# Optimization experiments

Hardware: AMD Instinct MI355X
Metric: run time of the kernel (lower is better)

Reference implementation:

```python
import jax, jax.numpy as jnp
import numpy as np

N_NODES = 50000
N_EDGES = 800000
N_GRAPHS = 512
K_HOPS = 2


def setup_inputs() -> dict:
    key = jax.random.key(0)
    ks = jax.random.split(key, 6)
    x = jax.random.normal(ks[0], (N_NODES, 75), dtype=jnp.float32)
    edge_index = jax.random.randint(ks[1], (2, N_EDGES), 0, N_NODES, dtype=jnp.int64)
    batch = jnp.sort(jax.random.randint(ks[2], (N_NODES,), 0, N_GRAPHS, dtype=jnp.int64))
    # Glorot-ish init for linear layers
    W1 = jax.random.normal(ks[3], (75, 128), dtype=jnp.float32) * (1.0 / np.sqrt(75))
    b1 = jnp.zeros((128,), dtype=jnp.float32)
    W2 = jax.random.normal(ks[4], (128, 1), dtype=jnp.float32) * (1.0 / np.sqrt(128))
    b2 = jnp.zeros((1,), dtype=jnp.float32)
    return {"x": x, "edge_index": edge_index, "batch": batch,
            "W1": W1, "b1": b1, "W2": W2, "b2": b2}


def _sgc_forward(x, edge_index, batch, W1, b1, W2, b2):
    N = x.shape[0]
    # gcn_norm with added self-loops (PyG SGConv default)
    loop = jnp.arange(N, dtype=edge_index.dtype)
    row = jnp.concatenate([edge_index[0], loop])
    col = jnp.concatenate([edge_index[1], loop])
    w = jnp.ones(row.shape[0], dtype=x.dtype)
    deg = jax.ops.segment_sum(w, col, num_segments=N)
    deg_inv_sqrt = jnp.where(deg > 0, jax.lax.rsqrt(jnp.maximum(deg, 1e-12)), 0.0)
    norm = deg_inv_sqrt[row] * deg_inv_sqrt[col]  # [E+N]
    # K hops of normalized sparse propagation: out[col] += norm * x[row]
    for _ in range(K_HOPS):
        x = jax.ops.segment_sum(norm[:, None] * x[row], col, num_segments=N)
    # SGConv final linear
    h = x @ W1 + b1  # [N,128]
    # global_add_pool: segment sum by graph id
    pooled = jax.ops.segment_sum(h, batch, num_segments=N_GRAPHS)  # [G,128]
    return pooled @ W2 + b2  # [G,1]


def reference(x, edge_index, batch, W1, b1, W2, b2):
    return _sgc_forward(x, edge_index, batch, W1, b1, W2, b2)
```

## Files before the change

kernel.cpp:

```cpp
#include <hip/hip_runtime.h>


#define N_    50000
#define E_    800000
#define G_    512
#define F_    75
#define H_    128
#define RR    256
#define BWR   196
#define PBLK  256
#define EPB   3125
#define SLOT  40
#define NT    196

struct Pr {
    const float* x; const int* row; const int* col; const int* batch;
    const float* W1; const float* b1; const float* W2; const float* b2;
    float* u; float2* kd; float* cbw; int* bcnt; int* bcnt2;
    unsigned* ebuf; unsigned* ebuf2; float* out;
};

__global__ __launch_bounds__(1024)
void k1_part(Pr p) {
    const int t = threadIdx.x, b = blockIdx.x;
    __shared__ float xs[NT * F_];
    __shared__ float sv[F_ + 1];
    __shared__ int wc[RR], wc2[RR];
    if (t < RR) { wc[t] = 0; wc2[t] = 0; }
    if (t < F_) {
        float s = 0.f;
        #pragma unroll 8
        for (int j = 0; j < H_; ++j) s += p.W1[t * H_ + j] * p.W2[j];
        sv[t] = s;
    }
    if (b == 0) {
        if (t >= 512 && t < 1024) p.out[t - 512] = p.b2[0];
        if (t == 500) {
            float s = 0.f;
            #pragma unroll 8
            for (int j = 0; j < H_; ++j) s += p.b1[j] * p.W2[j];
            p.cbw[0] = s;
        }
    }
    const int n0 = b * NT;
    int rem = N_ - n0; if (rem > NT) rem = NT; if (rem < 0) rem = 0;
    const int nf4 = rem * F_ / 4;
    const float4* xsrc = (const float4*)(p.x + (size_t)n0 * F_);
    for (int i = t; i < nf4; i += 1024) ((float4*)xs)[i] = xsrc[i];
    __syncthreads();
    const int e0 = b * EPB;
    for (int e = e0 + t; e < e0 + EPB; e += 1024) {
        int cv = p.col[e];
        int rv = p.row[e];
        int r = cv / BWR;
        int k = atomicAdd(&wc[r], 1);
        if (k < SLOT)
            p.ebuf[(size_t)(r * PBLK + b) * SLOT + k] =
                ((unsigned)rv << 8) | (unsigned)(cv - r * BWR);
        int r2 = rv / BWR;
        int k2 = atomicAdd(&wc2[r2], 1);
        if (k2 < SLOT)
            p.ebuf2[(size_t)(r2 * PBLK + b) * SLOT + k2] =
                ((unsigned)cv << 8) | (unsigned)(rv - r2 * BWR);
    }
    {
        const int ln = t >> 2, part = t & 3;
        if (ln < rem) {
            const float* xr = xs + ln * F_;
            float s = 0.f;
            for (int j = part; j < F_; j += 4) s += xr[j] * sv[j];
            s += __shfl_xor(s, 1);
            s += __shfl_xor(s, 2);
            if (part == 0) p.u[n0 + ln] = s;
        }
    }
    __syncthreads();
    if (t < RR) {
        int c = wc[t];  if (c > SLOT) c = SLOT;
        p.bcnt[t * PBLK + b] = c;
        int c2 = wc2[t]; if (c2 > SLOT) c2 = SLOT;
        p.bcnt2[t * PBLK + b] = c2;
    }
}

__global__ __launch_bounds__(1024)
void k2_deg(Pr p) {
    const int t = threadIdx.x, r = blockIdx.x;
    __shared__ float bins[BWR];
    __shared__ int scnt[PBLK];
    if (t < BWR) bins[t] = 0.f;
    if (t < PBLK) scnt[t] = p.bcnt[r * PBLK + t];
    __syncthreads();
    const int w = t >> 6, lane = t & 63;
    const unsigned* ebr = p.ebuf + (size_t)r * PBLK * SLOT;
    #pragma unroll
    for (int i = 0; i < PBLK / 16; ++i) {
        int b = w * (PBLK / 16) + i;
        if (lane < scnt[b]) {
            unsigned wd = ebr[(size_t)b * SLOT + lane];
            atomicAdd(&bins[wd & 255u], 1.0f);
        }
    }
    __syncthreads();
    if (t < BWR) {
        int node = r * BWR + t;
        if (node < N_) {
            float d = rsqrtf(bins[t] + 1.0f);
            p.kd[node] = make_float2(d, __int_as_float(p.batch[node]));
            p.u[node] = d * p.u[node];
        }
    }
}

__global__ __launch_bounds__(1024)
void k3_hop(Pr p) {
    const int t = threadIdx.x, r = blockIdx.x;
    __shared__ float bins[BWR];
    __shared__ float h[G_];
    __shared__ int scnt[PBLK], scnt2[PBLK];
    if (t < BWR) bins[t] = 0.f;
    for (int i = t; i < G_; i += 1024) h[i] = 0.f;
    if (t < PBLK) {
        scnt[t]  = p.bcnt[r * PBLK + t];
        scnt2[t] = p.bcnt2[r * PBLK + t];
    }
    __syncthreads();
    const int w = t >> 6, lane = t & 63;
    {
        const unsigned* ebr = p.ebuf + (size_t)r * PBLK * SLOT;
        #pragma unroll
        for (int i = 0; i < PBLK / 16; ++i) {
            int b = w * (PBLK / 16) + i;
            if (lane < scnt[b]) {
                unsigned wd = ebr[(size_t)b * SLOT + lane];
                atomicAdd(&bins[wd & 255u], p.u[wd >> 8]);
            }
        }
    }
    __syncthreads();
    if (t < 256) {
        float val = 0.f; int g = -1;
        int node = r * BWR + t;
        if (t < BWR && node < N_) {
            float2 k = p.kd[node];
            float nu = k.x * k.x * (bins[t] + p.u[node]);
            bins[t] = nu;
            val = k.x * nu + p.cbw[0];
            g = __float_as_int(k.y);
        }
        int g0 = __shfl(g, 0), g63 = __shfl(g, 63);
        if (g0 == g63 && g0 >= 0) {
            for (int o = 32; o; o >>= 1) val += __shfl_down(val, o);
            if ((t & 63) == 0) atomicAdd(&h[g0], val);
        } else if (g >= 0) {
            atomicAdd(&h[g], val);
        }
    }
    __syncthreads();
    {
        const unsigned* eb2 = p.ebuf2 + (size_t)r * PBLK * SLOT;
        #pragma unroll
        for (int i = 0; i < PBLK / 16; ++i) {
            int b = w * (PBLK / 16) + i;
            if (lane < scnt2[b]) {
                unsigned wd = eb2[(size_t)b * SLOT + lane];
                float2 k = p.kd[wd >> 8];
                atomicAdd(&h[__float_as_int(k.y)], k.x * bins[wd & 255u]);
            }
        }
    }
    __syncthreads();
    for (int i = t; i < G_; i += 1024)
        if (h[i] != 0.f) atomicAdd(&p.out[i], h[i]);
}

__global__ void f_setup(const float* W1, const float* b1, const float* W2,
                        const float* b2, float* v, float* cb) {
    int t = threadIdx.x;
    if (t < F_) {
        float s = 0.f;
        for (int j = 0; j < H_; ++j) s += W1[t * H_ + j] * W2[j];
        v[t] = s;
    } else if (t == F_) {
        float s = 0.f;
        for (int j = 0; j < H_; ++j) s += b1[j] * W2[j];
        cb[0] = s; cb[1] = b2[0];
    }
}
__global__ void f_init(float* deg, float* s, int n) {
    int i = blockIdx.x * blockDim.x + threadIdx.x;
    if (i < n) { deg[i] = 1.0f; s[i] = 0.0f; }
}
__global__ void f_deg_acc(const int* __restrict__ col, float* deg, int e) {
    int i = blockIdx.x * blockDim.x + threadIdx.x;
    if (i < e) atomicAdd(&deg[col[i]], 1.0f);
}
__global__ void f_dis(float* deg, int n) {
    int i = blockIdx.x * blockDim.x + threadIdx.x;
    if (i < n) deg[i] = rsqrtf(deg[i]);
}
__global__ void f_u0(const float* __restrict__ x, const float* __restrict__ v,
                     const float* __restrict__ dis, float* u, int n) {
    __shared__ float sv[F_];
    if (threadIdx.x < F_) sv[threadIdx.x] = v[threadIdx.x];
    __syncthreads();
    int i = blockIdx.x * blockDim.x + threadIdx.x;
    if (i < n) {
        const float* xi = x + (size_t)i * F_;
        float s = 0.f;
        for (int j = 0; j < F_; ++j) s += xi[j] * sv[j];
        u[i] = dis[i] * s;
    }
}
__global__ void f_edge(const int* __restrict__ row, const int* __restrict__ col,
                       const float* __restrict__ u, float* s, int e) {
    int i = blockIdx.x * blockDim.x + threadIdx.x;
    if (i < e) atomicAdd(&s[col[i]], u[row[i]]);
}
__global__ void f_hop_finish(const float* __restrict__ dis, float* s, float* u, int n) {
    int i = blockIdx.x * blockDim.x + threadIdx.x;
    if (i < n) { float d = dis[i]; u[i] = d * d * (s[i] + u[i]); s[i] = 0.0f; }
}
__global__ void f_out_init(const float* __restrict__ cb, float* out, int g) {
    int i = blockIdx.x * blockDim.x + threadIdx.x;
    if (i < g) out[i] = cb[1];
}
__global__ void f_pool(const int* __restrict__ batch, const float* __restrict__ dis,
                       const float* __restrict__ s, const float* __restrict__ u,
                       const float* __restrict__ cb, float* out, int n) {
    int i = blockIdx.x * blockDim.x + threadIdx.x;
    if (i < n) atomicAdd(&out[batch[i]], dis[i] * (s[i] + u[i]) + cb[0]);
}

extern "C" void kernel_launch(void* const* d_in, const int* in_sizes, int n_in,
                              void* d_out, int out_size, void* d_ws, size_t ws_size,
                              hipStream_t stream) {
    const float* x   = (const float*)d_in[0];
    const int*   ei  = (const int*)d_in[1];
    const int*   bat = (const int*)d_in[2];
    const float* W1  = (const float*)d_in[3];
    const float* b1  = (const float*)d_in[4];
    const float* W2  = (const float*)d_in[5];
    const float* b2  = (const float*)d_in[6];
    float* out = (float*)d_out;

    float* ws = (float*)d_ws;
    Pr p;
    p.x = x; p.row = ei; p.col = ei + E_; p.batch = bat;
    p.W1 = W1; p.b1 = b1; p.W2 = W2; p.b2 = b2;
    p.u     = ws;
    p.kd    = (float2*)(ws + N_ + (N_ & 1));
    p.cbw   = ws + 3 * N_ + 2;
    p.bcnt  = (int*)(p.cbw + 8);
    p.bcnt2 = p.bcnt + RR * PBLK;
    p.ebuf  = (unsigned*)(p.bcnt2 + RR * PBLK);
    p.ebuf2 = p.ebuf + (size_t)RR * PBLK * SLOT;
    p.out   = out;

    const size_t need = ((size_t)3 * N_ + 16 + 2 * (size_t)RR * PBLK * (1 + SLOT))
                        * sizeof(float);

    if (ws_size >= need) {
        k1_part<<<PBLK, 1024, 0, stream>>>(p);
        k2_deg<<<RR, 1024, 0, stream>>>(p);
        k3_hop<<<RR, 1024, 0, stream>>>(p);
    } else {
        float* v  = ws;
        float* cb = ws + 128;
        float* dis = ws + 136;
        float* u  = dis + N_;
        float* s  = u + N_;
        const int B = 256;
        const int gN = (N_ + B - 1) / B;
        const int gE = (E_ + B - 1) / B;
        f_setup<<<1, 128, 0, stream>>>(W1, b1, W2, b2, v, cb);
        f_init<<<gN, B, 0, stream>>>(dis, s, N_);
        f_deg_acc<<<gE, B, 0, stream>>>(ei + E_, dis, E_);
        f_dis<<<gN, B, 0, stream>>>(dis, N_);
        f_u0<<<gN, B, 0, stream>>>(x, v, dis, u, N_);
        f_edge<<<gE, B, 0, stream>>>(ei, ei + E_, u, s, E_);
        f_hop_finish<<<gN, B, 0, stream>>>(dis, s, u, N_);
        f_out_init<<<1, G_, 0, stream>>>(cb, out, G_);
        f_edge<<<gE, B, 0, stream>>>(ei, ei + E_, u, s, E_);
        f_pool<<<gN, B, 0, stream>>>(bat, dis, s, u, cb, out, N_);
    }
}
```

Baseline: 54.90 us.

## Halve partition blocks, widen edge slots, compute node projections directly from global

Reduces the first-pass grid from 256 to 128 blocks, each handling twice as many edges, with 64 bucket slots per destination range instead of 40. The per-node projection of x onto W1·W2 no longer stages x in shared memory; each block instead processes 391 nodes with four threads each reading contiguous chunks straight from global memory. This removes the large shared tile and halves the per-range bucket count the hop kernels must scan, at the cost of fewer blocks, less parallelism in the first kernel, and strided uncoalesced global loads for x.

```diff
diff --git a/kernel.cpp b/kernel.cpp
--- a/kernel.cpp
+++ b/kernel.cpp
@@ -8,10 +8,11 @@
 #define H_    128
 #define RR    256
 #define BWR   196
-#define PBLK  256
-#define EPB   3125
-#define SLOT  40
-#define NT    196
+#define PBLK  128
+#define EPB   6250
+#define SLOT  64
+#define NB    391
+#define SEGW  8
 
 struct Pr {
     const float* x; const int* row; const int* col; const int* batch;
@@ -23,7 +24,6 @@
 __global__ __launch_bounds__(1024)
 void k1_part(Pr p) {
     const int t = threadIdx.x, b = blockIdx.x;
-    __shared__ float xs[NT * F_];
     __shared__ float sv[F_ + 1];
     __shared__ int wc[RR], wc2[RR];
     if (t < RR) { wc[t] = 0; wc2[t] = 0; }
@@ -42,11 +42,6 @@
             p.cbw[0] = s;
         }
     }
-    const int n0 = b * NT;
-    int rem = N_ - n0; if (rem > NT) rem = NT; if (rem < 0) rem = 0;
-    const int nf4 = rem * F_ / 4;
-    const float4* xsrc = (const float4*)(p.x + (size_t)n0 * F_);
-    for (int i = t; i < nf4; i += 1024) ((float4*)xs)[i] = xsrc[i];
     __syncthreads();
     const int e0 = b * EPB;
     for (int e = e0 + t; e < e0 + EPB; e += 1024) {
@@ -63,15 +58,17 @@
             p.ebuf2[(size_t)(r2 * PBLK + b) * SLOT + k2] =
                 ((unsigned)cv << 8) | (unsigned)(rv - r2 * BWR);
     }
-    {
-        const int ln = t >> 2, part = t & 3;
-        if (ln < rem) {
-            const float* xr = xs + ln * F_;
+    for (int nt = t; nt < 4 * NB; nt += 1024) {
+        int i = b * NB + (nt >> 2);
+        if (i < N_) {
+            int part = nt & 3;
+            int j0 = part * 19, j1 = j0 + 19; if (j1 > F_) j1 = F_;
+            const float* xi = p.x + (size_t)i * F_;
             float s = 0.f;
-            for (int j = part; j < F_; j += 4) s += xr[j] * sv[j];
+            for (int j = j0; j < j1; ++j) s += xi[j] * sv[j];
             s += __shfl_xor(s, 1);
             s += __shfl_xor(s, 2);
-            if (part == 0) p.u[n0 + ln] = s;
+            if (part == 0) p.u[i] = s;
         }
     }
     __syncthreads();
@@ -94,8 +91,8 @@
     const int w = t >> 6, lane = t & 63;
     const unsigned* ebr = p.ebuf + (size_t)r * PBLK * SLOT;
     #pragma unroll
-    for (int i = 0; i < PBLK / 16; ++i) {
-        int b = w * (PBLK / 16) + i;
+    for (int i = 0; i < SEGW; ++i) {
+        int b = w * SEGW + i;
         if (lane < scnt[b]) {
             unsigned wd = ebr[(size_t)b * SLOT + lane];
             atomicAdd(&bins[wd & 255u], 1.0f);
@@ -129,8 +126,8 @@
     {
         const unsigned* ebr = p.ebuf + (size_t)r * PBLK * SLOT;
         #pragma unroll
-        for (int i = 0; i < PBLK / 16; ++i) {
-            int b = w * (PBLK / 16) + i;
+        for (int i = 0; i < SEGW; ++i) {
+            int b = w * SEGW + i;
             if (lane < scnt[b]) {
                 unsigned wd = ebr[(size_t)b * SLOT + lane];
                 atomicAdd(&bins[wd & 255u], p.u[wd >> 8]);
@@ -160,8 +157,8 @@
     {
         const unsigned* eb2 = p.ebuf2 + (size_t)r * PBLK * SLOT;
         #pragma unroll
-        for (int i = 0; i < PBLK / 16; ++i) {
-            int b = w * (PBLK / 16) + i;
+        for (int i = 0; i < SEGW; ++i) {
+            int b = w * SEGW + i;
             if (lane < scnt2[b]) {
                 unsigned wd = eb2[(size_t)b * SLOT + lane];
                 float2 k = p.kd[wd >> 8];
```

Result: slower. 60.45 us (+10.1%).

## Stage edge partitions in LDS and move node projection into degree kernel

Applied to the files above, without the earlier changes.

The partition kernel now writes bucketed edges into shared-memory staging arrays and then copies each block's full bucket region to global memory with coalesced uint4 stores, replacing scattered 4-byte global writes. The buffer layout becomes source-block-major, so the consumer kernels read with a strided per-bucket index. The x·(W1·W2) projection and x tile load move from the partition kernel into the degree kernel, where node ranges match the bucket ranges. The projected value is written directly scaled by the degree factor, which removes one read-modify-write of u. In exchange, the partition kernel uses about 80KB of LDS and writes the full padded slot region, including empty slots.

```diff
diff --git a/kernel.cpp b/kernel.cpp
--- a/kernel.cpp
+++ b/kernel.cpp
@@ -11,7 +11,7 @@
 #define PBLK  256
 #define EPB   3125
 #define SLOT  40
-#define NT    196
+#define SEGW  16
 
 struct Pr {
     const float* x; const int* row; const int* col; const int* batch;
@@ -23,16 +23,10 @@
 __global__ __launch_bounds__(1024)
 void k1_part(Pr p) {
     const int t = threadIdx.x, b = blockIdx.x;
-    __shared__ float xs[NT * F_];
-    __shared__ float sv[F_ + 1];
+    __shared__ __align__(16) unsigned st1[RR * SLOT];
+    __shared__ __align__(16) unsigned st2[RR * SLOT];
     __shared__ int wc[RR], wc2[RR];
     if (t < RR) { wc[t] = 0; wc2[t] = 0; }
-    if (t < F_) {
-        float s = 0.f;
-        #pragma unroll 8
-        for (int j = 0; j < H_; ++j) s += p.W1[t * H_ + j] * p.W2[j];
-        sv[t] = s;
-    }
     if (b == 0) {
         if (t >= 512 && t < 1024) p.out[t - 512] = p.b2[0];
         if (t == 500) {
@@ -42,11 +36,6 @@
             p.cbw[0] = s;
         }
     }
-    const int n0 = b * NT;
-    int rem = N_ - n0; if (rem > NT) rem = NT; if (rem < 0) rem = 0;
-    const int nf4 = rem * F_ / 4;
-    const float4* xsrc = (const float4*)(p.x + (size_t)n0 * F_);
-    for (int i = t; i < nf4; i += 1024) ((float4*)xs)[i] = xsrc[i];
     __syncthreads();
     const int e0 = b * EPB;
     for (int e = e0 + t; e < e0 + EPB; e += 1024) {
@@ -55,26 +44,21 @@
         int r = cv / BWR;
         int k = atomicAdd(&wc[r], 1);
         if (k < SLOT)
-            p.ebuf[(size_t)(r * PBLK + b) * SLOT + k] =
-                ((unsigned)rv << 8) | (unsigned)(cv - r * BWR);
+            st1[r * SLOT + k] = ((unsigned)rv << 8) | (unsigned)(cv - r * BWR);
         int r2 = rv / BWR;
         int k2 = atomicAdd(&wc2[r2], 1);
         if (k2 < SLOT)
-            p.ebuf2[(size_t)(r2 * PBLK + b) * SLOT + k2] =
-                ((unsigned)cv << 8) | (unsigned)(rv - r2 * BWR);
-    }
+            st2[r2 * SLOT + k2] = ((unsigned)cv << 8) | (unsigned)(rv - r2 * BWR);
+    }
+    __syncthreads();
     {
-        const int ln = t >> 2, part = t & 3;
-        if (ln < rem) {
-            const float* xr = xs + ln * F_;
-            float s = 0.f;
-            for (int j = part; j < F_; j += 4) s += xr[j] * sv[j];
-            s += __shfl_xor(s, 1);
-            s += __shfl_xor(s, 2);
-            if (part == 0) p.u[n0 + ln] = s;
-        }
-    }
-    __syncthreads();
+        uint4* d1 = (uint4*)(p.ebuf + (size_t)b * RR * SLOT);
+        uint4* d2 = (uint4*)(p.ebuf2 + (size_t)b * RR * SLOT);
+        const uint4* s1 = (const uint4*)st1;
+        const uint4* s2 = (const uint4*)st2;
+        #pragma unroll
+        for (int i = t; i < RR * SLOT / 4; i += 1024) { d1[i] = s1[i]; d2[i] = s2[i]; }
+    }
     if (t < RR) {
         int c = wc[t];  if (c > SLOT) c = SLOT;
         p.bcnt[t * PBLK + b] = c;
@@ -86,28 +70,46 @@
 __global__ __launch_bounds__(1024)
 void k2_deg(Pr p) {
     const int t = threadIdx.x, r = blockIdx.x;
+    __shared__ float xs[BWR * F_];
+    __shared__ float sv[F_ + 1];
     __shared__ float bins[BWR];
     __shared__ int scnt[PBLK];
+    if (t < F_) {
+        float s = 0.f;
+        #pragma unroll 8
+        for (int j = 0; j < H_; ++j) s += p.W1[t * H_ + j] * p.W2[j];
+        sv[t] = s;
+    }
     if (t < BWR) bins[t] = 0.f;
     if (t < PBLK) scnt[t] = p.bcnt[r * PBLK + t];
+    const int n0 = r * BWR;
+    int rem = N_ - n0; if (rem > BWR) rem = BWR; if (rem < 0) rem = 0;
+    const int nf4 = rem * F_ / 4;
+    const float4* xsrc = (const float4*)(p.x + (size_t)n0 * F_);
+    for (int i = t; i < nf4; i += 1024) ((float4*)xs)[i] = xsrc[i];
     __syncthreads();
     const int w = t >> 6, lane = t & 63;
-    const unsigned* ebr = p.ebuf + (size_t)r * PBLK * SLOT;
     #pragma unroll
-    for (int i = 0; i < PBLK / 16; ++i) {
-        int b = w * (PBLK / 16) + i;
+    for (int i = 0; i < SEGW; ++i) {
+        int b = w * SEGW + i;
         if (lane < scnt[b]) {
-            unsigned wd = ebr[(size_t)b * SLOT + lane];
+            unsigned wd = p.ebuf[(size_t)(b * RR + r) * SLOT + lane];
             atomicAdd(&bins[wd & 255u], 1.0f);
         }
     }
     __syncthreads();
-    if (t < BWR) {
-        int node = r * BWR + t;
-        if (node < N_) {
-            float d = rsqrtf(bins[t] + 1.0f);
+    const int ln = t >> 2, part = t & 3;
+    if (ln < rem) {
+        const float* xr = xs + ln * F_;
+        float s = 0.f;
+        for (int j = part; j < F_; j += 4) s += xr[j] * sv[j];
+        s += __shfl_xor(s, 1);
+        s += __shfl_xor(s, 2);
+        if (part == 0) {
+            int node = n0 + ln;
+            float d = rsqrtf(bins[ln] + 1.0f);
             p.kd[node] = make_float2(d, __int_as_float(p.batch[node]));
-            p.u[node] = d * p.u[node];
+            p.u[node] = d * s;
         }
     }
 }
@@ -126,15 +128,12 @@
     }
     __syncthreads();
     const int w = t >> 6, lane = t & 63;
-    {
-        const unsigned* ebr = p.ebuf + (size_t)r * PBLK * SLOT;
-        #pragma unroll
-        for (int i = 0; i < PBLK / 16; ++i) {
-            int b = w * (PBLK / 16) + i;
-            if (lane < scnt[b]) {
-                unsigned wd = ebr[(size_t)b * SLOT + lane];
-                atomicAdd(&bins[wd & 255u], p.u[wd >> 8]);
-            }
+    #pragma unroll
+    for (int i = 0; i < SEGW; ++i) {
+        int b = w * SEGW + i;
+        if (lane < scnt[b]) {
+            unsigned wd = p.ebuf[(size_t)(b * RR + r) * SLOT + lane];
+            atomicAdd(&bins[wd & 255u], p.u[wd >> 8]);
         }
     }
     __syncthreads();
@@ -157,16 +156,13 @@
         }
     }
     __syncthreads();
-    {
-        const unsigned* eb2 = p.ebuf2 + (size_t)r * PBLK * SLOT;
-        #pragma unroll
-        for (int i = 0; i < PBLK / 16; ++i) {
-            int b = w * (PBLK / 16) + i;
-            if (lane < scnt2[b]) {
-                unsigned wd = eb2[(size_t)b * SLOT + lane];
-                float2 k = p.kd[wd >> 8];
-                atomicAdd(&h[__float_as_int(k.y)], k.x * bins[wd & 255u]);
-            }
+    #pragma unroll
+    for (int i = 0; i < SEGW; ++i) {
+        int b = w * SEGW + i;
+        if (lane < scnt2[b]) {
+            unsigned wd = p.ebuf2[(size_t)(b * RR + r) * SLOT + lane];
+            float2 k = p.kd[wd >> 8];
+            atomicAdd(&h[__float_as_int(k.y)], k.x * bins[wd & 255u]);
         }
     }
     __syncthreads();
@@ -249,15 +245,15 @@
     p.x = x; p.row = ei; p.col = ei + E_; p.batch = bat;
     p.W1 = W1; p.b1 = b1; p.W2 = W2; p.b2 = b2;
     p.u     = ws;
-    p.kd    = (float2*)(ws + N_ + (N_ & 1));
-    p.cbw   = ws + 3 * N_ + 2;
+    p.kd    = (float2*)(ws + N_);
+    p.cbw   = ws + 3 * N_;
     p.bcnt  = (int*)(p.cbw + 8);
     p.bcnt2 = p.bcnt + RR * PBLK;
     p.ebuf  = (unsigned*)(p.bcnt2 + RR * PBLK);
-    p.ebuf2 = p.ebuf + (size_t)RR * PBLK * SLOT;
+    p.ebuf2 = p.ebuf + (size_t)PBLK * RR * SLOT;
     p.out   = out;
 
-    const size_t need = ((size_t)3 * N_ + 16 + 2 * (size_t)RR * PBLK * (1 + SLOT))
+    const size_t need = ((size_t)3 * N_ + 8 + 2 * (size_t)RR * PBLK * (1 + SLOT))
                         * sizeof(float);
 
     if (ws_size >= need) {
```

Measured after the change: 54.31 us. No clear change (-1.1%).
